# Kernel tuning notes

Measured on AMD Instinct MI355X. Metric: run time of the kernel, lower is better.

## Reference

```python
import jax, jax.numpy as jnp
import numpy as np
from jax import lax

B, S, IN, H, C = 128, 128, 512, 256, 256  # batch, num_sentences, word_hidden*2, sentence_hidden, context
BN_EPS = 1e-5


def setup_inputs() -> dict:
    key = jax.random.key(0)
    ks = jax.random.split(key, 16)
    u = lambda k, shape: jax.random.uniform(k, shape, minval=-0.1, maxval=0.1, dtype=jnp.float32)
    return {
        "x": jax.random.normal(ks[0], (B, S, IN), jnp.float32),
        "sent_hidden_stat": jnp.zeros((2, B, H), jnp.float32),  # unused by forward (as in original)
        "num_sentences_lens": jax.random.randint(ks[1], (B,), 1, S + 1),
        # bidirectional GRU weights (PyTorch layout: [3H, in], gate order r,z,n)
        "w_ih_f": u(ks[2], (3 * H, IN)), "w_hh_f": u(ks[3], (3 * H, H)),
        "b_ih_f": u(ks[4], (3 * H,)),   "b_hh_f": u(ks[5], (3 * H,)),
        "w_ih_b": u(ks[6], (3 * H, IN)), "w_hh_b": u(ks[7], (3 * H, H)),
        "b_ih_b": u(ks[8], (3 * H,)),   "b_hh_b": u(ks[9], (3 * H,)),
        # sentence projection Linear(2H -> C)
        "proj_w": u(ks[10], (C, 2 * H)), "proj_b": u(ks[11], (C,)),
        # BatchNorm1d(num_features=S) affine params
        "bn_gamma": jnp.ones((S,), jnp.float32), "bn_beta": jnp.zeros((S,), jnp.float32),
        # sentence context vector [C, 1]
        "context": u(ks[12], (C, 1)),
    }


def _gru_dir(x, w_ih, w_hh, b_ih, b_hh):
    """Single-direction GRU over x: [B, T, IN] -> [B, T, H] (PyTorch GRU math)."""
    Hd = w_hh.shape[1]
    xp = jnp.einsum('bti,gi->tbg', x, w_ih) + b_ih  # [T, B, 3H], input projections precomputed

    def step(h, xpt):
        hp = h @ w_hh.T + b_hh
        xr, xz, xn = jnp.split(xpt, 3, axis=-1)
        hr, hz, hn = jnp.split(hp, 3, axis=-1)
        r = jax.nn.sigmoid(xr + hr)
        z = jax.nn.sigmoid(xz + hz)
        n = jnp.tanh(xn + r * hn)
        h_new = (1.0 - z) * n + z * h
        return h_new, h_new

    h0 = jnp.zeros((x.shape[0], Hd), x.dtype)
    _, ys = lax.scan(step, h0, xp)
    return jnp.swapaxes(ys, 0, 1)  # [B, T, H]


def reference(x, sent_hidden_stat, num_sentences_lens,
              w_ih_f, w_hh_f, b_ih_f, b_hh_f,
              w_ih_b, w_hh_b, b_ih_b, b_hh_b,
              proj_w, proj_b, bn_gamma, bn_beta, context):
    # Bidirectional GRU over sentences
    out_f = _gru_dir(x, w_ih_f, w_hh_f, b_ih_f, b_hh_f)
    out_b = _gru_dir(x[:, ::-1], w_ih_b, w_hh_b, b_ih_b, b_hh_b)[:, ::-1]
    out = jnp.concatenate([out_f, out_b], axis=-1)  # [B, S, 2H]

    # _fetch/get_mask: zero out positions beyond each document's sentence count
    mask = (jnp.arange(out.shape[1])[None, :] < num_sentences_lens[:, None]).astype(out.dtype)
    out = out * mask[:, :, None]

    # projection -> BatchNorm1d(num_features=S, training stats) -> ReLU
    proj = jnp.einsum('bsd,cd->bsc', out, proj_w) + proj_b  # [B, S, C]
    mu = proj.mean(axis=(0, 2), keepdims=True)
    var = jnp.mean((proj - mu) ** 2, axis=(0, 2), keepdims=True)
    bn = (proj - mu) / jnp.sqrt(var + BN_EPS) * bn_gamma[None, :, None] + bn_beta[None, :, None]
    p = jax.nn.relu(bn)

    # additive attention pooling over sentences
    scores = jnp.einsum('bsc,co->bs', p, context)  # [B, S]
    attn = jax.nn.softmax(scores, axis=1)
    return jnp.einsum('bs,bsd->bd', attn, out)  # [B, 2H]
```

## Files before the change

### kernel.cpp

```cpp
#include <hip/hip_runtime.h>
#include <hip/hip_bf16.h>

#define B_   128
#define S_   128
#define IN_  512
#define H_   256
#define G3_  768
#define C_   256
#define D2H_ 512
#define XPAD 20

typedef short bf16x8 __attribute__((ext_vector_type(8)));
typedef float f32x4  __attribute__((ext_vector_type(4)));

static __device__ __forceinline__ short f2bf(float f) {
  unsigned u = __float_as_uint(f);
  return (short)((u + 0x7fffu + ((u >> 16) & 1u)) >> 16);
}
static __device__ __forceinline__ float bf2f(unsigned short v) {
  return __uint_as_float((unsigned)v << 16);
}

static __device__ __forceinline__ void async16(const void* g, const void* l) {
  __builtin_amdgcn_global_load_lds(
      (const __attribute__((address_space(1))) void*)g,
      (__attribute__((address_space(3))) void*)l, 16, 0, 0);
}

__global__ __launch_bounds__(256) void xp_gemm_bf(
    const float* __restrict__ x,
    const float* __restrict__ wf, const float* __restrict__ wb,
    const float* __restrict__ bif, const float* __restrict__ bhf,
    const float* __restrict__ bib, const float* __restrict__ bhb,
    unsigned short* __restrict__ xpf, unsigned short* __restrict__ xpb)
{
  const int sb = blockIdx.x;
  const int bn = blockIdx.y;
  const bool fwd = (bn < 6);
  const float* __restrict__ wsrc = fwd ? wf : wb;
  const float* __restrict__ bi   = fwd ? bif : bib;
  const float* __restrict__ bh   = fwd ? bhf : bhb;
  const int nloc0 = (fwd ? bn : bn - 6) * 128;

  __shared__ __align__(16) unsigned short As[128][56];
  __shared__ __align__(16) unsigned short Bs[128][56];

  const int tid  = threadIdx.x;
  const int wave = tid >> 6, lane = tid & 63;
  const int col  = lane & 15, lg = lane >> 4;
  const int wm   = wave >> 1, wn = wave & 1;
  const int rr   = tid >> 1;
  const int hf   = (tid & 1) * 16;

  const float* ax = x    + ((size_t)(rr * 128 + sb) * IN_ + hf);
  const float* bx = wsrc + ((size_t)(nloc0 + rr) * IN_ + hf);

  f32x4 acc[4][4];
#pragma unroll
  for (int i = 0; i < 4; ++i)
#pragma unroll
    for (int j = 0; j < 4; ++j) acc[i][j] = f32x4{0.f, 0.f, 0.f, 0.f};

  for (int k0 = 0; k0 < IN_; k0 += 32) {
    float4 a0 = *(const float4*)(ax + k0);
    float4 a1 = *(const float4*)(ax + k0 + 4);
    float4 a2 = *(const float4*)(ax + k0 + 8);
    float4 a3 = *(const float4*)(ax + k0 + 12);
    float4 c0 = *(const float4*)(bx + k0);
    float4 c1 = *(const float4*)(bx + k0 + 4);
    float4 c2 = *(const float4*)(bx + k0 + 8);
    float4 c3 = *(const float4*)(bx + k0 + 12);
    __syncthreads();
    {
      bf16x8 p0, p1;
      p0[0]=f2bf(a0.x); p0[1]=f2bf(a0.y); p0[2]=f2bf(a0.z); p0[3]=f2bf(a0.w);
      p0[4]=f2bf(a1.x); p0[5]=f2bf(a1.y); p0[6]=f2bf(a1.z); p0[7]=f2bf(a1.w);
      p1[0]=f2bf(a2.x); p1[1]=f2bf(a2.y); p1[2]=f2bf(a2.z); p1[3]=f2bf(a2.w);
      p1[4]=f2bf(a3.x); p1[5]=f2bf(a3.y); p1[6]=f2bf(a3.z); p1[7]=f2bf(a3.w);
      *(bf16x8*)&As[rr][hf]     = p0;
      *(bf16x8*)&As[rr][hf + 8] = p1;
      p0[0]=f2bf(c0.x); p0[1]=f2bf(c0.y); p0[2]=f2bf(c0.z); p0[3]=f2bf(c0.w);
      p0[4]=f2bf(c1.x); p0[5]=f2bf(c1.y); p0[6]=f2bf(c1.z); p0[7]=f2bf(c1.w);
      p1[0]=f2bf(c2.x); p1[1]=f2bf(c2.y); p1[2]=f2bf(c2.z); p1[3]=f2bf(c2.w);
      p1[4]=f2bf(c3.x); p1[5]=f2bf(c3.y); p1[6]=f2bf(c3.z); p1[7]=f2bf(c3.w);
      *(bf16x8*)&Bs[rr][hf]     = p0;
      *(bf16x8*)&Bs[rr][hf + 8] = p1;
    }
    __syncthreads();
    bf16x8 af[4], bf_[4];
#pragma unroll
    for (int mi = 0; mi < 4; ++mi)
      af[mi] = *(const bf16x8*)&As[wm * 64 + mi * 16 + col][lg * 8];
#pragma unroll
    for (int ni = 0; ni < 4; ++ni)
      bf_[ni] = *(const bf16x8*)&Bs[wn * 64 + ni * 16 + col][lg * 8];
#pragma unroll
    for (int mi = 0; mi < 4; ++mi)
#pragma unroll
      for (int ni = 0; ni < 4; ++ni)
        acc[mi][ni] = __builtin_amdgcn_mfma_f32_16x16x32_bf16(af[mi], bf_[ni], acc[mi][ni], 0, 0, 0);
  }

  const int t = fwd ? sb : (S_ - 1 - sb);
  unsigned short* __restrict__ dstbase = fwd ? xpf : xpb;
#pragma unroll
  for (int ni = 0; ni < 4; ++ni) {
    const int g = nloc0 + wn * 64 + ni * 16 + col;
    const float bias = bi[g] + (g < 2 * H_ ? bh[g] : 0.f);
#pragma unroll
    for (int mi = 0; mi < 4; ++mi) {
      const int grp = wm * 4 + mi;
      ushort4 o;
      o.x = (unsigned short)f2bf(acc[mi][ni][0] + bias);
      o.y = (unsigned short)f2bf(acc[mi][ni][1] + bias);
      o.z = (unsigned short)f2bf(acc[mi][ni][2] + bias);
      o.w = (unsigned short)f2bf(acc[mi][ni][3] + bias);
      *(ushort4*)(dstbase + (((size_t)t * 8 + grp) * G3_ + g) * XPAD + lg * 4) = o;
    }
  }
}

__global__ __launch_bounds__(512, 2) void gru_mfma(
    const unsigned short* __restrict__ xpf, const unsigned short* __restrict__ xpb,
    const float* __restrict__ whf, const float* __restrict__ whb,
    const float* __restrict__ bhf, const float* __restrict__ bhb,
    const int* __restrict__ lens, float* __restrict__ out)
{
  const int dir = blockIdx.x >> 3;
  const int grp = blockIdx.x & 7;
  const int b0  = grp * 16;
  const unsigned short* __restrict__ xp = dir ? xpb : xpf;
  const float* __restrict__ whh = dir ? whb : whf;
  const float* __restrict__ bhh = dir ? bhb : bhf;

  const int tid  = threadIdx.x;
  const int wave = tid >> 6;
  const int lane = tid & 63;
  const int col  = lane & 15;
  const int lg   = lane >> 4;
  const int gb0  = wave * 32 + col;

  __shared__ __align__(16) unsigned short hlds[2][32][16][8];
  __shared__ __align__(16) unsigned short xlds[2][G3_ * XPAD];

  ((int4*)&hlds[0][0][0][0])[tid] = int4{0, 0, 0, 0};

  {
    const unsigned short* base = xp + (size_t)grp * (G3_ * XPAD);
    const char* lb = (const char*)&xlds[0][0];
#pragma unroll
    for (int j = 0; j < 4; ++j) {
      const int c = j * 512 + tid;
      if (c < 1920)
        async16(base + (size_t)c * 8, lb + (size_t)(j * 512 + wave * 64) * 16);
    }
  }

  bf16x8 wfg[2][3][8];
#pragma unroll
  for (int tt = 0; tt < 2; ++tt) {
    const int gbase = gb0 + tt * 16;
#pragma unroll
    for (int g = 0; g < 3; ++g) {
      const float* wrow = whh + (size_t)(g * H_ + gbase) * H_;
#pragma unroll
      for (int kk = 0; kk < 8; ++kk) {
        const float* p = wrow + kk * 32 + lg * 8;
        float4 w0 = *(const float4*)p;
        float4 w1 = *(const float4*)(p + 4);
        bf16x8 f;
        f[0] = f2bf(w0.x); f[1] = f2bf(w0.y); f[2] = f2bf(w0.z); f[3] = f2bf(w0.w);
        f[4] = f2bf(w1.x); f[5] = f2bf(w1.y); f[6] = f2bf(w1.z); f[7] = f2bf(w1.w);
        wfg[tt][g][kk] = f;
      }
    }
  }

  float bhn[2];
  bhn[0] = bhh[2 * H_ + gb0];
  bhn[1] = bhh[2 * H_ + gb0 + 16];

  int len_[4];
#pragma unroll
  for (int i = 0; i < 4; ++i) len_[i] = lens[b0 + lg * 4 + i];

  float hreg[2][4] = {};

  int p = 0;
  for (int t = 0; t < S_; ++t) {
    __syncthreads();
    const int xb = t & 1;

    if (t + 1 < S_) {
      const unsigned short* base = xp + ((size_t)(t + 1) * 8 + grp) * (G3_ * XPAD);
      const char* lb = (const char*)&xlds[xb ^ 1][0];
#pragma unroll
      for (int j = 0; j < 4; ++j) {
        const int c = j * 512 + tid;
        if (c < 1920)
          async16(base + (size_t)c * 8, lb + (size_t)(j * 512 + wave * 64) * 16);
      }
    }

    const int s_out = dir ? (S_ - 1 - t) : t;

#pragma unroll
    for (int tt = 0; tt < 2; ++tt) {
      const int u = gb0 + tt * 16;
      ushort4 r4 = *(const ushort4*)&xlds[xb][(size_t)u * XPAD + lg * 4];
      ushort4 z4 = *(const ushort4*)&xlds[xb][(size_t)(H_ + u) * XPAD + lg * 4];
      f32x4 accr, accz, accn;
      accr[0] = bf2f(r4.x); accr[1] = bf2f(r4.y); accr[2] = bf2f(r4.z); accr[3] = bf2f(r4.w);
      accz[0] = bf2f(z4.x); accz[1] = bf2f(z4.y); accz[2] = bf2f(z4.z); accz[3] = bf2f(z4.w);
      accn = f32x4{bhn[tt], bhn[tt], bhn[tt], bhn[tt]};
#pragma unroll
      for (int kk = 0; kk < 8; ++kk) {
        bf16x8 a = *(const bf16x8*)&hlds[p][kk * 4 + lg][col][0];
        accr = __builtin_amdgcn_mfma_f32_16x16x32_bf16(a, wfg[tt][0][kk], accr, 0, 0, 0);
        accz = __builtin_amdgcn_mfma_f32_16x16x32_bf16(a, wfg[tt][1][kk], accz, 0, 0, 0);
        accn = __builtin_amdgcn_mfma_f32_16x16x32_bf16(a, wfg[tt][2][kk], accn, 0, 0, 0);
      }
      ushort4 n4 = *(const ushort4*)&xlds[xb][(size_t)(2 * H_ + u) * XPAD + lg * 4];
#pragma unroll
      for (int i = 0; i < 4; ++i) {
        const int bi = lg * 4 + i;
        float r  = 1.f / (1.f + __expf(-accr[i]));
        float z  = 1.f / (1.f + __expf(-accz[i]));
        float nx = bf2f((&n4.x)[i]) + r * accn[i];
        float n  = 1.f - 2.f / (__expf(2.f * nx) + 1.f);
        float hn = n + z * (hreg[tt][i] - n);
        hreg[tt][i] = hn;
        out[((size_t)(b0 + bi) * S_ + s_out) * D2H_ + dir * H_ + u] =
            (s_out < len_[i]) ? hn : 0.f;
        hlds[p ^ 1][u >> 3][bi][u & 7] = (unsigned short)f2bf(hn);
      }
    }
    p ^= 1;
  }
}

__global__ __launch_bounds__(256) void proj_gemm(
    const float* __restrict__ a, const float* __restrict__ w,
    const float* __restrict__ bias, float* __restrict__ proj)
{
  const int bm = blockIdx.x;
  const int n0 = blockIdx.y * 64;

  __shared__ float As[16][68];
  __shared__ float Bs[16][68];

  const int tid = threadIdx.x;
  const int row = tid >> 2;
  const int kq  = (tid & 3) << 2;
  const int tx  = tid & 15, ty = tid >> 4;

  const float* arow = a + (size_t)(bm * 64 + row) * D2H_ + kq;
  const float* brow = w + (size_t)(n0 + row) * D2H_ + kq;

  float acc[4][4] = {};

  for (int k0 = 0; k0 < D2H_; k0 += 16) {
    float4 av = *(const float4*)(arow + k0);
    float4 bv = *(const float4*)(brow + k0);
    As[kq + 0][row] = av.x; As[kq + 1][row] = av.y;
    As[kq + 2][row] = av.z; As[kq + 3][row] = av.w;
    Bs[kq + 0][row] = bv.x; Bs[kq + 1][row] = bv.y;
    Bs[kq + 2][row] = bv.z; Bs[kq + 3][row] = bv.w;
    __syncthreads();
#pragma unroll
    for (int k = 0; k < 16; ++k) {
      float4 av2 = *(const float4*)&As[k][ty * 4];
      float4 bv2 = *(const float4*)&Bs[k][tx * 4];
      acc[0][0] += av2.x * bv2.x; acc[0][1] += av2.x * bv2.y; acc[0][2] += av2.x * bv2.z; acc[0][3] += av2.x * bv2.w;
      acc[1][0] += av2.y * bv2.x; acc[1][1] += av2.y * bv2.y; acc[1][2] += av2.y * bv2.z; acc[1][3] += av2.y * bv2.w;
      acc[2][0] += av2.z * bv2.x; acc[2][1] += av2.z * bv2.y; acc[2][2] += av2.z * bv2.z; acc[2][3] += av2.z * bv2.w;
      acc[3][0] += av2.w * bv2.x; acc[3][1] += av2.w * bv2.y; acc[3][2] += av2.w * bv2.z; acc[3][3] += av2.w * bv2.w;
    }
    __syncthreads();
  }

  float4 bv4 = *(const float4*)(bias + n0 + tx * 4);
#pragma unroll
  for (int i = 0; i < 4; ++i) {
    int m = bm * 64 + ty * 4 + i;
    float4 o;
    o.x = acc[i][0] + bv4.x; o.y = acc[i][1] + bv4.y;
    o.z = acc[i][2] + bv4.z; o.w = acc[i][3] + bv4.w;
    *(float4*)(proj + (size_t)m * C_ + n0 + tx * 4) = o;
  }
}

__global__ __launch_bounds__(256) void bn_stats(
    const float* __restrict__ proj, float* __restrict__ mu, float* __restrict__ rstd)
{
  const int s = blockIdx.x, tid = threadIdx.x;
  float sum = 0.f, sq = 0.f;
  for (int b = 0; b < B_; ++b) {
    float v = proj[((size_t)b * S_ + s) * C_ + tid];
    sum += v; sq += v * v;
  }
#pragma unroll
  for (int o = 32; o; o >>= 1) { sum += __shfl_down(sum, o); sq += __shfl_down(sq, o); }
  __shared__ float r1[4], r2[4];
  const int lane = tid & 63, wid = tid >> 6;
  if (!lane) { r1[wid] = sum; r2[wid] = sq; }
  __syncthreads();
  if (!tid) {
    float s1 = r1[0] + r1[1] + r1[2] + r1[3];
    float s2 = r2[0] + r2[1] + r2[2] + r2[3];
    float m = s1 / (float)(B_ * C_);
    float var = s2 / (float)(B_ * C_) - m * m;
    mu[s] = m;
    rstd[s] = rsqrtf(var + 1e-5f);
  }
}

__global__ __launch_bounds__(256) void score_k(
    const float* __restrict__ proj, const float* __restrict__ mu,
    const float* __restrict__ rstd, const float* __restrict__ gamma,
    const float* __restrict__ beta, const float* __restrict__ ctx,
    float* __restrict__ scores)
{
  const int wid = threadIdx.x >> 6, lane = threadIdx.x & 63;
  const int m = blockIdx.x * 4 + wid;
  const int s = m & 127;
  float4 v  = *(const float4*)(proj + (size_t)m * C_ + lane * 4);
  float4 cv = *(const float4*)(ctx + lane * 4);
  const float ms = mu[s], rs = rstd[s], g = gamma[s], be = beta[s];
  float acc = fmaxf((v.x - ms) * rs * g + be, 0.f) * cv.x
            + fmaxf((v.y - ms) * rs * g + be, 0.f) * cv.y
            + fmaxf((v.z - ms) * rs * g + be, 0.f) * cv.z
            + fmaxf((v.w - ms) * rs * g + be, 0.f) * cv.w;
#pragma unroll
  for (int o = 32; o; o >>= 1) acc += __shfl_down(acc, o);
  if (!lane) scores[m] = acc;
}

__global__ __launch_bounds__(128) void softmax_k(
    const float* __restrict__ scores, float* __restrict__ attn)
{
  const int b = blockIdx.x, tid = threadIdx.x;
  float v = scores[b * S_ + tid];
  float mx = v;
#pragma unroll
  for (int o = 32; o; o >>= 1) mx = fmaxf(mx, __shfl_down(mx, o));
  __shared__ float t0[2], t1[2];
  const int lane = tid & 63, wid = tid >> 6;
  if (!lane) t0[wid] = mx;
  __syncthreads();
  mx = fmaxf(t0[0], t0[1]);
  float e = __expf(v - mx);
  float ssum = e;
#pragma unroll
  for (int o = 32; o; o >>= 1) ssum += __shfl_down(ssum, o);
  if (!lane) t1[wid] = ssum;
  __syncthreads();
  attn[b * S_ + tid] = e / (t1[0] + t1[1]);
}

__global__ __launch_bounds__(512) void final_k(
    const float* __restrict__ attn, const float* __restrict__ out,
    float* __restrict__ y)
{
  const int b = blockIdx.x, d = threadIdx.x;
  __shared__ float a[S_];
  if (threadIdx.x < S_) a[threadIdx.x] = attn[b * S_ + threadIdx.x];
  __syncthreads();
  float acc = 0.f;
  for (int s = 0; s < S_; ++s)
    acc += a[s] * out[((size_t)b * S_ + s) * D2H_ + d];
  y[(size_t)b * D2H_ + d] = acc;
}

extern "C" void kernel_launch(void* const* d_in, const int* in_sizes, int n_in,
                              void* d_out, int out_size, void* d_ws, size_t ws_size,
                              hipStream_t stream)
{
  const float* x      = (const float*)d_in[0];
  const int*   lens   = (const int*)d_in[2];
  const float* w_ih_f = (const float*)d_in[3];
  const float* w_hh_f = (const float*)d_in[4];
  const float* b_ih_f = (const float*)d_in[5];
  const float* b_hh_f = (const float*)d_in[6];
  const float* w_ih_b = (const float*)d_in[7];
  const float* w_hh_b = (const float*)d_in[8];
  const float* b_ih_b = (const float*)d_in[9];
  const float* b_hh_b = (const float*)d_in[10];
  const float* proj_w = (const float*)d_in[11];
  const float* proj_b = (const float*)d_in[12];
  const float* gamma  = (const float*)d_in[13];
  const float* beta   = (const float*)d_in[14];
  const float* ctx    = (const float*)d_in[15];

  float* ws = (float*)d_ws;
  float* outm = ws;
  unsigned short* xpf = (unsigned short*)(ws + 8388608);
  unsigned short* xpb = xpf + 15728640;
  float* proj   = ws + 8388608;
  float* mu     = ws + 12582912;
  float* rstd   = ws + 12583040;
  float* scores = ws + 12583168;
  float* attn   = ws + 12599552;

  xp_gemm_bf<<<dim3(128, 12), 256, 0, stream>>>(
      x, w_ih_f, w_ih_b, b_ih_f, b_hh_f, b_ih_b, b_hh_b, xpf, xpb);
  gru_mfma<<<16, 512, 0, stream>>>(xpf, xpb, w_hh_f, w_hh_b, b_hh_f, b_hh_b, lens, outm);
  proj_gemm<<<dim3(256, 4), 256, 0, stream>>>(outm, proj_w, proj_b, proj);
  bn_stats<<<128, 256, 0, stream>>>(proj, mu, rstd);
  score_k<<<4096, 256, 0, stream>>>(proj, mu, rstd, gamma, beta, ctx, scores);
  softmax_k<<<128, 128, 0, stream>>>(scores, attn);
  final_k<<<128, 512, 0, stream>>>(attn, outm, (float*)d_out);
}
```

Before: 548.0 us.

## Stream n-gate recurrent weights from packed buffer and defer masked output stores

Adds a pack kernel that converts the n-gate recurrent weights to bf16 in MFMA fragment order, and the GRU kernel now reloads them from global/L2 every step instead of holding them in registers. This cuts register pressure in the latency-bound recurrence. Output stores are deferred by one step and use precomputed pointers, and the bf16 packing of the hidden state uses v_cvt_pk_bf16_f32. The cost is extra per-step global loads on the critical serial path and an additional small kernel launch.

```diff
diff --git a/kernel.cpp b/kernel.cpp
--- a/kernel.cpp
+++ b/kernel.cpp
@@ -25,6 +25,23 @@
   __builtin_amdgcn_global_load_lds(
       (const __attribute__((address_space(1))) void*)g,
       (__attribute__((address_space(3))) void*)l, 16, 0, 0);
+}
+
+__global__ __launch_bounds__(1024) void pack_wn(
+    const float* __restrict__ whf, const float* __restrict__ whb,
+    unsigned short* __restrict__ wnp)
+{
+  const int o = blockIdx.x * 1024 + threadIdx.x;
+  const int j    = o & 7;
+  const int lane = (o >> 3) & 63;
+  const int kk   = (o >> 9) & 7;
+  const int tt   = (o >> 12) & 1;
+  const int wave = (o >> 13) & 7;
+  const int dir  = (o >> 16) & 1;
+  const float* w = dir ? whb : whf;
+  const int row = wave * 32 + tt * 16 + (lane & 15);
+  const int k   = kk * 32 + (lane >> 4) * 8 + j;
+  wnp[o] = (unsigned short)f2bf(w[(size_t)(2 * H_ + row) * H_ + k]);
 }
 
 __global__ __launch_bounds__(256) void xp_gemm_bf(
@@ -87,18 +104,18 @@
       *(bf16x8*)&Bs[rr][hf + 8] = p1;
     }
     __syncthreads();
-    bf16x8 af[4], bf_[4];
+    bf16x8 af[4], bfv[4];
 #pragma unroll
     for (int mi = 0; mi < 4; ++mi)
       af[mi] = *(const bf16x8*)&As[wm * 64 + mi * 16 + col][lg * 8];
 #pragma unroll
     for (int ni = 0; ni < 4; ++ni)
-      bf_[ni] = *(const bf16x8*)&Bs[wn * 64 + ni * 16 + col][lg * 8];
+      bfv[ni] = *(const bf16x8*)&Bs[wn * 64 + ni * 16 + col][lg * 8];
 #pragma unroll
     for (int mi = 0; mi < 4; ++mi)
 #pragma unroll
       for (int ni = 0; ni < 4; ++ni)
-        acc[mi][ni] = __builtin_amdgcn_mfma_f32_16x16x32_bf16(af[mi], bf_[ni], acc[mi][ni], 0, 0, 0);
+        acc[mi][ni] = __builtin_amdgcn_mfma_f32_16x16x32_bf16(af[mi], bfv[ni], acc[mi][ni], 0, 0, 0);
   }
 
   const int t = fwd ? sb : (S_ - 1 - sb);
@@ -124,6 +141,7 @@
     const unsigned short* __restrict__ xpf, const unsigned short* __restrict__ xpb,
     const float* __restrict__ whf, const float* __restrict__ whb,
     const float* __restrict__ bhf, const float* __restrict__ bhb,
+    const unsigned short* __restrict__ wnp,
     const int* __restrict__ lens, float* __restrict__ out)
 {
   const int dir = blockIdx.x >> 3;
@@ -156,25 +174,27 @@
     }
   }
 
-  bf16x8 wfg[2][3][8];
+  bf16x8 wrz[2][2][8];
 #pragma unroll
   for (int tt = 0; tt < 2; ++tt) {
     const int gbase = gb0 + tt * 16;
 #pragma unroll
-    for (int g = 0; g < 3; ++g) {
+    for (int g = 0; g < 2; ++g) {
       const float* wrow = whh + (size_t)(g * H_ + gbase) * H_;
 #pragma unroll
       for (int kk = 0; kk < 8; ++kk) {
-        const float* p = wrow + kk * 32 + lg * 8;
-        float4 w0 = *(const float4*)p;
-        float4 w1 = *(const float4*)(p + 4);
+        const float* pw = wrow + kk * 32 + lg * 8;
+        float4 w0 = *(const float4*)pw;
+        float4 w1 = *(const float4*)(pw + 4);
         bf16x8 f;
         f[0] = f2bf(w0.x); f[1] = f2bf(w0.y); f[2] = f2bf(w0.z); f[3] = f2bf(w0.w);
         f[4] = f2bf(w1.x); f[5] = f2bf(w1.y); f[6] = f2bf(w1.z); f[7] = f2bf(w1.w);
-        wfg[tt][g][kk] = f;
+        wrz[tt][g][kk] = f;
       }
     }
   }
+
+  const unsigned short* wnb = wnp + ((size_t)(dir * 8 + wave) << 13) + lane * 8;
 
   float bhn[2];
   bhn[0] = bhh[2 * H_ + gb0];
@@ -185,11 +205,36 @@
   for (int i = 0; i < 4; ++i) len_[i] = lens[b0 + lg * 4 + i];
 
   float hreg[2][4] = {};
+
+  const int s0 = dir ? (S_ - 1) : 0;
+  float* op[4];
+#pragma unroll
+  for (int i = 0; i < 4; ++i)
+    op[i] = out + ((size_t)(b0 + lg * 4 + i) * S_ + s0) * D2H_ + dir * H_ + gb0;
+  const ptrdiff_t sdelta = dir ? -(ptrdiff_t)D2H_ : (ptrdiff_t)D2H_;
 
   int p = 0;
   for (int t = 0; t < S_; ++t) {
     __syncthreads();
     const int xb = t & 1;
+
+    bf16x8 wn[2][8];
+#pragma unroll
+    for (int tt = 0; tt < 2; ++tt)
+#pragma unroll
+      for (int kk = 0; kk < 8; ++kk)
+        wn[tt][kk] = *(const bf16x8*)(wnb + ((tt * 8 + kk) << 9));
+
+    if (t > 0) {
+      const int s_prev = dir ? (S_ - t) : (t - 1);
+#pragma unroll
+      for (int i = 0; i < 4; ++i) {
+        const bool m = s_prev < len_[i];
+        op[i][0]  = m ? hreg[0][i] : 0.f;
+        op[i][16] = m ? hreg[1][i] : 0.f;
+        op[i] += sdelta;
+      }
+    }
 
     if (t + 1 < S_) {
       const unsigned short* base = xp + ((size_t)(t + 1) * 8 + grp) * (G3_ * XPAD);
@@ -201,8 +246,6 @@
           async16(base + (size_t)c * 8, lb + (size_t)(j * 512 + wave * 64) * 16);
       }
     }
-
-    const int s_out = dir ? (S_ - 1 - t) : t;
 
 #pragma unroll
     for (int tt = 0; tt < 2; ++tt) {
@@ -216,26 +259,42 @@
 #pragma unroll
       for (int kk = 0; kk < 8; ++kk) {
         bf16x8 a = *(const bf16x8*)&hlds[p][kk * 4 + lg][col][0];
-        accr = __builtin_amdgcn_mfma_f32_16x16x32_bf16(a, wfg[tt][0][kk], accr, 0, 0, 0);
-        accz = __builtin_amdgcn_mfma_f32_16x16x32_bf16(a, wfg[tt][1][kk], accz, 0, 0, 0);
-        accn = __builtin_amdgcn_mfma_f32_16x16x32_bf16(a, wfg[tt][2][kk], accn, 0, 0, 0);
+        accr = __builtin_amdgcn_mfma_f32_16x16x32_bf16(a, wrz[tt][0][kk], accr, 0, 0, 0);
+        accz = __builtin_amdgcn_mfma_f32_16x16x32_bf16(a, wrz[tt][1][kk], accz, 0, 0, 0);
+        accn = __builtin_amdgcn_mfma_f32_16x16x32_bf16(a, wn[tt][kk], accn, 0, 0, 0);
       }
       ushort4 n4 = *(const ushort4*)&xlds[xb][(size_t)(2 * H_ + u) * XPAD + lg * 4];
+      float hnv[4];
 #pragma unroll
       for (int i = 0; i < 4; ++i) {
-        const int bi = lg * 4 + i;
         float r  = 1.f / (1.f + __expf(-accr[i]));
         float z  = 1.f / (1.f + __expf(-accz[i]));
         float nx = bf2f((&n4.x)[i]) + r * accn[i];
         float n  = 1.f - 2.f / (__expf(2.f * nx) + 1.f);
         float hn = n + z * (hreg[tt][i] - n);
         hreg[tt][i] = hn;
-        out[((size_t)(b0 + bi) * S_ + s_out) * D2H_ + dir * H_ + u] =
-            (s_out < len_[i]) ? hn : 0.f;
-        hlds[p ^ 1][u >> 3][bi][u & 7] = (unsigned short)f2bf(hn);
+        hnv[i] = hn;
       }
+      unsigned pk01, pk23;
+      asm("v_cvt_pk_bf16_f32 %0, %1, %2" : "=v"(pk01) : "v"(hnv[0]), "v"(hnv[1]));
+      asm("v_cvt_pk_bf16_f32 %0, %1, %2" : "=v"(pk23) : "v"(hnv[2]), "v"(hnv[3]));
+      const int kb = u >> 3, jj = u & 7;
+      hlds[p ^ 1][kb][lg * 4 + 0][jj] = (unsigned short)(pk01 & 0xffffu);
+      hlds[p ^ 1][kb][lg * 4 + 1][jj] = (unsigned short)(pk01 >> 16);
+      hlds[p ^ 1][kb][lg * 4 + 2][jj] = (unsigned short)(pk23 & 0xffffu);
+      hlds[p ^ 1][kb][lg * 4 + 3][jj] = (unsigned short)(pk23 >> 16);
     }
     p ^= 1;
+  }
+
+  {
+    const int s_last = dir ? 0 : (S_ - 1);
+#pragma unroll
+    for (int i = 0; i < 4; ++i) {
+      const bool m = s_last < len_[i];
+      op[i][0]  = m ? hreg[0][i] : 0.f;
+      op[i][16] = m ? hreg[1][i] : 0.f;
+    }
   }
 }
 
@@ -396,15 +455,18 @@
   float* outm = ws;
   unsigned short* xpf = (unsigned short*)(ws + 8388608);
   unsigned short* xpb = xpf + 15728640;
+  unsigned short* wnp = xpb + 15728640;
   float* proj   = ws + 8388608;
   float* mu     = ws + 12582912;
   float* rstd   = ws + 12583040;
   float* scores = ws + 12583168;
   float* attn   = ws + 12599552;
 
+  pack_wn<<<128, 1024, 0, stream>>>(w_hh_f, w_hh_b, wnp);
   xp_gemm_bf<<<dim3(128, 12), 256, 0, stream>>>(
       x, w_ih_f, w_ih_b, b_ih_f, b_hh_f, b_ih_b, b_hh_b, xpf, xpb);
-  gru_mfma<<<16, 512, 0, stream>>>(xpf, xpb, w_hh_f, w_hh_b, b_hh_f, b_hh_b, lens, outm);
+  gru_mfma<<<16, 512, 0, stream>>>(xpf, xpb, w_hh_f, w_hh_b, b_hh_f, b_hh_b,
+                                   wnp, lens, outm);
   proj_gemm<<<dim3(256, 4), 256, 0, stream>>>(outm, proj_w, proj_b, proj);
   bn_stats<<<128, 256, 0, stream>>>(proj, mu, rstd);
   score_k<<<4096, 256, 0, stream>>>(proj, mu, rstd, gamma, beta, ctx, scores);
```

Result: slower. 566.6 us (+3.4%).
